# Kernel optimization log

Measured on AMD Instinct MI355X. Metric: run time of the kernel, lower is better.

The kernel has to match this reference:

```python
import jax, jax.numpy as jnp
import numpy as np

L, D, DB, P, B = 33, 2048, 1024, 24, 2048
EPS = 1e-5

def _ln(x, g, b):
    # LayerNorm over last axis, eps matches torch default 1e-5
    mu = jnp.mean(x, axis=-1, keepdims=True)
    var = jnp.mean(jnp.square(x - mu), axis=-1, keepdims=True)
    return (x - mu) * jax.lax.rsqrt(var + EPS) * g + b

def setup_inputs() -> dict:
    key = jax.random.key(0)
    ks = jax.random.split(key, 8)
    s1 = 1.0 / np.sqrt(D)   # fan-in style scaling to keep activations sane
    s2 = 1.0 / np.sqrt(DB)
    sp = 1.0 / np.sqrt(P)
    return {
        "x":      jax.random.normal(ks[0], (B, L, D), jnp.float32),
        "pos_emb": jax.random.uniform(ks[1], (L, P), jnp.float32),
        "Wk":     jax.random.normal(ks[2], (P, D), jnp.float32) * sp,
        "W1":     jax.random.normal(ks[3], (L, D, DB), jnp.float32) * s1,
        "b1":     jnp.zeros((L, DB), jnp.float32),
        "ln1_g":  jnp.ones((L, DB), jnp.float32),
        "ln1_b":  jnp.zeros((L, DB), jnp.float32),
        "W2":     jax.random.normal(ks[4], (L, DB, D), jnp.float32) * s2,
        "b2":     jnp.zeros((L, D), jnp.float32),
        "ln2_g":  jnp.ones((L, D), jnp.float32),
        "ln2_b":  jnp.zeros((L, D), jnp.float32),
        "Wq1":    jax.random.normal(ks[5], (D, DB), jnp.float32) * s1,
        "bq1":    jnp.zeros((DB,), jnp.float32),
        "lnq_g":  jnp.ones((DB,), jnp.float32),
        "lnq_b":  jnp.zeros((DB,), jnp.float32),
        "Wq2":    jax.random.normal(ks[6], (DB, D), jnp.float32) * s2,
        "bq2":    jnp.zeros((D,), jnp.float32),
    }

def reference(x, pos_emb, Wk, W1, b1, ln1_g, ln1_b, W2, b2, ln2_g, ln2_b,
              Wq1, bq1, lnq_g, lnq_b, Wq2, bq2):
    # x: [B, L, D]
    z_L = x[:, -1, :]                                   # [B, D]
    keys = pos_emb @ Wk                                 # Eq.10: [L, D]
    # Eq.11 + Eq.4: per-layer value MLPs, grouped as batched GEMMs
    h = jax.nn.gelu(jnp.einsum('bld,ldk->blk', x, W1) + b1, approximate=False)
    h = _ln(h, ln1_g, ln1_b)                            # [B, L, DB]
    v = jnp.einsum('blk,lkd->bld', h, W2) + b2          # [B, L, D]
    values = _ln(v, ln2_g, ln2_b)                       # [B, L, D]
    # Eq.5: query from last layer
    hq = jax.nn.gelu(z_L @ Wq1 + bq1, approximate=False)
    hq = _ln(hq, lnq_g, lnq_b)
    q_tr = hq @ Wq2 + bq2                               # [B, D]
    query = 1.0 + jax.nn.elu(z_L + q_tr)                # [B, D]
    # Eq.7-9: single-query attention over depth + residual
    attn = jax.nn.softmax(query @ keys.T, axis=-1)      # [B, L]
    attended = jnp.einsum('bl,bld->bd', attn, values)   # [B, D]
    return z_L + attended
```

## Files before the change

kernel.cpp:

```cpp
#include <hip/hip_runtime.h>
#include <cstddef>
#include <cstdint>

#define Lc 33
#define Dc 2048
#define DBc 1024
#define Pc 24
#define Bc 2048

typedef __attribute__((ext_vector_type(4))) float f32x4;
typedef __attribute__((ext_vector_type(8))) short s16x8;
typedef __attribute__((ext_vector_type(4))) short s16x4;

__device__ __forceinline__ short bf16r(float f) {
  unsigned u = __float_as_uint(f);
  u = (u + 0x7fffu + ((u >> 16) & 1u)) >> 16;
  return (short)u;
}
__device__ __forceinline__ float bf2f(short s) {
  return __uint_as_float(((unsigned)(unsigned short)s) << 16);
}
__device__ __forceinline__ s16x8 pack8(const float* f) {
  s16x8 r;
#pragma unroll
  for (int i = 0; i < 8; ++i) r[i] = bf16r(f[i]);
  return r;
}
__device__ __forceinline__ void split8(const float* f, s16x8& hi, s16x8& lo) {
#pragma unroll
  for (int i = 0; i < 8; ++i) {
    short h = bf16r(f[i]);
    hi[i] = h;
    lo[i] = bf16r(f[i] - bf2f(h));
  }
}
__device__ __forceinline__ void gl_lds16(const void* g, void* l) {
  __builtin_amdgcn_global_load_lds(
      (const __attribute__((address_space(1))) unsigned int*)g,
      (__attribute__((address_space(3))) unsigned int*)l, 16, 0, 0);
}

#define BARw() __builtin_amdgcn_s_barrier()
#define VM4() asm volatile("s_waitcnt vmcnt(4)" ::: "memory")

__global__ __launch_bounds__(256)
void cvt_bf16_kernel(const float* __restrict__ in,
                     unsigned short* __restrict__ outp) {
  const size_t i = ((size_t)blockIdx.x * 256 + threadIdx.x) * 8;
  f32x4 a = *(const f32x4*)(in + i);
  f32x4 b = *(const f32x4*)(in + i + 4);
  float f[8] = {a[0], a[1], a[2], a[3], b[0], b[1], b[2], b[3]};
  *(s16x8*)(outp + i) = pack8(f);
}

__global__ __launch_bounds__(256)
void keys_kernel(const float* __restrict__ pe, const float* __restrict__ Wk,
                 float* __restrict__ keys) {
  const int l = blockIdx.x;
  const int d = blockIdx.y * 256 + threadIdx.x;
  float s = 0.f;
#pragma unroll
  for (int p = 0; p < Pc; ++p) s += pe[l * Pc + p] * Wk[(size_t)p * Dc + d];
  keys[(size_t)l * Dc + d] = s;
}

template <int K, int N>
__global__ __launch_bounds__(256)
void transpose_w(const float* __restrict__ W, unsigned short* __restrict__ Wt) {
  const int z = blockIdx.z;
  const int k0 = blockIdx.x * 64, n0 = blockIdx.y * 64;
  __shared__ unsigned short tile[64][66];
  const int t = threadIdx.x;
  {
    const int r = t >> 2, cq = (t & 3) * 16;
    const float* src = W + (size_t)z * K * N + (size_t)(k0 + r) * N + n0 + cq;
#pragma unroll
    for (int i = 0; i < 16; i += 4) {
      f32x4 v = *(const f32x4*)(src + i);
#pragma unroll
      for (int j = 0; j < 4; ++j)
        tile[r][cq + i + j] = (unsigned short)bf16r(v[j]);
    }
  }
  __syncthreads();
  {
    const int n = t >> 2, kc = (t & 3) * 16;
    s16x8 o0, o1;
#pragma unroll
    for (int i = 0; i < 8; ++i) {
      o0[i] = tile[kc + i][n];
      o1[i] = tile[kc + 8 + i][n];
    }
    unsigned short* dst =
        Wt + (size_t)z * N * K + (size_t)(n0 + n) * K + k0 + kc;
    *(s16x8*)dst = o0;
    *(s16x8*)(dst + 8) = o1;
  }
}

template <int K, int N, int NBN, int GELU, int STATS>
__global__ __launch_bounds__(512, 2)
void gemm8ph(const unsigned short* __restrict__ A,
             const unsigned short* __restrict__ Wt,
             const float* __restrict__ bias,
             unsigned short* __restrict__ outbuf, float* __restrict__ stats) {
  constexpr int NT = K / 64;
  constexpr int NIT = NT / 2;
  constexpr int NBM = 8;
  extern __shared__ __align__(16) char smem[];

  constexpr int nwg = 33 * NBM * NBN;
  constexpr int q = nwg >> 3, r = nwg & 7;
  const int orig = blockIdx.x;
  const int xcd = orig & 7;
  const int wgid =
      ((xcd < r) ? xcd * (q + 1) : r * (q + 1) + (xcd - r) * q) + (orig >> 3);
  const int z = wgid / (NBM * NBN);
  const int rem = wgid - z * (NBM * NBN);
  const int bm = rem / NBN, bn = rem - bm * NBN;

  const int tid = threadIdx.x, lane = tid & 63, wv = tid >> 6;
  const int wm = wv >> 2, wn = wv & 3;
  const int wr = wm * 128, wc = wn * 64;
  const int l15 = lane & 15, l4 = lane >> 4;

  f32x4 acc[8][4];
#pragma unroll
  for (int m = 0; m < 8; ++m)
#pragma unroll
    for (int n = 0; n < 4; ++n) {
      acc[m][n][0] = 0.f; acc[m][n][1] = 0.f;
      acc[m][n][2] = 0.f; acc[m][n][3] = 0.f;
    }

  const unsigned short* aRow[2];
  const unsigned short* bRow[2];
  {
    const unsigned short* Bbase = Wt + (size_t)z * N * K;
#pragma unroll
    for (int c = 0; c < 2; ++c) {
      const int rprime = wv * 16 + c * 8 + (lane >> 3);
      const int row = 2 * rprime + ((lane >> 2) & 1);
      const int chunk = (lane & 3) ^ (rprime & 3);
      aRow[c] = A + (size_t)(bm * 256 + row) * ((size_t)Lc * K) +
                (size_t)z * K + chunk * 8;
      bRow[c] = Bbase + (size_t)(bn * 256 + row) * K + chunk * 8;
    }
  }

  auto STAGE_A = [&](int t, int kh) {
    char* dst = smem + (t & 1) * 65536 + kh * 16384 + wv * 2048;
    const int ko = t * 64 + kh * 32;
#pragma unroll
    for (int c = 0; c < 2; ++c) gl_lds16(aRow[c] + ko, dst + c * 1024);
  };
  auto STAGE_B = [&](int t, int kh) {
    char* dst = smem + (t & 1) * 65536 + 32768 + kh * 16384 + wv * 2048;
    const int ko = t * 64 + kh * 32;
#pragma unroll
    for (int c = 0; c < 2; ++c) gl_lds16(bRow[c] + ko, dst + c * 1024);
  };
  s16x8 afr[4], bfr[4];
  auto LDA = [&](int d, int kh, int mh) {
#pragma unroll
    for (int m = 0; m < 4; ++m) {
      const int row = wr + (mh * 4 + m) * 16 + l15;
      const int rp = row >> 1;
      afr[m] = *(const s16x8*)(smem + d * 65536 + kh * 16384 + rp * 128 +
                               (row & 1) * 64 + ((l4 ^ (rp & 3)) << 4));
    }
  };
  auto LDB = [&](int d, int kh) {
#pragma unroll
    for (int n = 0; n < 4; ++n) {
      const int row = wc + n * 16 + l15;
      const int rp = row >> 1;
      bfr[n] = *(const s16x8*)(smem + d * 65536 + 32768 + kh * 16384 +
                               rp * 128 + (row & 1) * 64 +
                               ((l4 ^ (rp & 3)) << 4));
    }
  };

#define MFMA16(MH)                                                          \
  {                                                                         \
    __builtin_amdgcn_s_setprio(1);                                          \
    _Pragma("unroll") for (int m_ = 0; m_ < 4; ++m_) {                      \
      _Pragma("unroll") for (int n_ = 0; n_ < 4; ++n_) {                    \
        acc[(MH) * 4 + m_][n_] = __builtin_amdgcn_mfma_f32_16x16x32_bf16(   \
            afr[m_], bfr[n_], acc[(MH) * 4 + m_][n_], 0, 0, 0);             \
      }                                                                     \
    }                                                                       \
    __builtin_amdgcn_s_setprio(0);                                          \
  }

  STAGE_A(0, 0); STAGE_B(0, 0); STAGE_A(0, 1); STAGE_B(0, 1);
  STAGE_A(1, 0); STAGE_B(1, 0);
  VM4();
  BARw();

  for (int i = 0; i < NIT; ++i) {
    const int t0 = 2 * i, t1 = 2 * i + 1;
    LDA(0, 0, 0); LDB(0, 0);
    STAGE_A(t1, 1);
    BARw(); MFMA16(0); BARw();
    LDA(0, 0, 1);
    STAGE_B(t1, 1);
    BARw(); MFMA16(1); BARw();
    LDA(0, 1, 0); LDB(0, 1);
    if (t0 + 2 < NT) STAGE_A(t0 + 2, 0);
    BARw(); MFMA16(0); BARw();
    LDA(0, 1, 1);
    if (t0 + 2 < NT) STAGE_B(t0 + 2, 0);
    BARw(); MFMA16(1);
    VM4();
    BARw();
    LDA(1, 0, 0); LDB(1, 0);
    if (t0 + 2 < NT) STAGE_A(t0 + 2, 1);
    BARw(); MFMA16(0); BARw();
    LDA(1, 0, 1);
    if (t0 + 2 < NT) STAGE_B(t0 + 2, 1);
    BARw(); MFMA16(1); BARw();
    LDA(1, 1, 0); LDB(1, 1);
    if (t0 + 3 < NT) STAGE_A(t0 + 3, 0);
    BARw(); MFMA16(0); BARw();
    LDA(1, 1, 1);
    if (t0 + 3 < NT) STAGE_B(t0 + 3, 0);
    BARw(); MFMA16(1);
    VM4();
    BARw();
  }
#undef MFMA16

  const float* biasP = bias + (size_t)z * N;
  float bsv[4];
#pragma unroll
  for (int n = 0; n < 4; ++n) bsv[n] = biasP[bn * 256 + wc + n * 16 + l15];

#pragma unroll
  for (int m = 0; m < 8; ++m) {
#pragma unroll
    for (int j = 0; j < 4; ++j) {
      const int grow = bm * 256 + wr + m * 16 + l4 * 4 + j;
      float s1 = 0.f, s2 = 0.f;
#pragma unroll
      for (int n = 0; n < 4; ++n) {
        const int col = bn * 256 + wc + n * 16 + l15;
        float v = acc[m][n][j] + bsv[n];
        if constexpr (GELU) v = 0.5f * v * (1.0f + erff(v * 0.70710678118f));
        outbuf[((size_t)grow * Lc + z) * N + col] = (unsigned short)bf16r(v);
        if constexpr (STATS) {
          s1 += v;
          s2 += v * v;
        }
      }
      if constexpr (STATS) {
#pragma unroll
        for (int o = 1; o < 16; o <<= 1) {
          s1 += __shfl_xor(s1, o);
          s2 += __shfl_xor(s2, o);
        }
        if (l15 == 0) {
          atomicAdd(&stats[((size_t)grow * Lc + z) * 2 + 0], s1);
          atomicAdd(&stats[((size_t)grow * Lc + z) * 2 + 1], s2);
        }
      }
    }
  }
}

template <int K, int N, int GELU>
__global__ __launch_bounds__(256, 2)
void gemm2ph(const unsigned short* __restrict__ A,
             const unsigned short* __restrict__ Wt,
             const float* __restrict__ bias,
             unsigned short* __restrict__ outbuf) {
  constexpr int NT = K / 64;
  const int z = blockIdx.z, bm = blockIdx.x, bn = blockIdx.y;
  const int tid = threadIdx.x, lane = tid & 63, w = tid >> 6;
  const int wr = (w >> 1) * 64, wc = (w & 1) * 64;
  const int l15 = lane & 15, kb = lane >> 4;

  __shared__ __align__(16) unsigned short Als[2][128 * 64];
  __shared__ __align__(16) unsigned short Bls[2][128 * 64];

  f32x4 acc[4][4];
#pragma unroll
  for (int m = 0; m < 4; ++m)
#pragma unroll
    for (int n = 0; n < 4; ++n) {
      acc[m][n][0] = 0.f; acc[m][n][1] = 0.f;
      acc[m][n][2] = 0.f; acc[m][n][3] = 0.f;
    }

  const int rl8 = lane >> 3, sl = lane & 7;
  const int swzE = ((sl ^ rl8) << 3);
  const unsigned short* Bbase = Wt + (size_t)z * N * K;

  auto stage = [&](int buf, int kt) {
#pragma unroll
    for (int j = 0; j < 4; ++j) {
      const int rloc = w * 32 + j * 8 + rl8;
      gl_lds16(A + ((size_t)(bm * 128 + rloc) * Lc + z) * K + kt * 64 + swzE,
               (char*)&Als[buf][0] + w * 4096 + j * 1024);
      gl_lds16(Bbase + (size_t)(bn * 128 + rloc) * K + kt * 64 + swzE,
               (char*)&Bls[buf][0] + w * 4096 + j * 1024);
    }
  };

  stage(0, 0);
  asm volatile("s_waitcnt vmcnt(0)" ::: "memory");
  __builtin_amdgcn_s_barrier();

  for (int kt = 0; kt < NT; ++kt) {
    const int cur = kt & 1;
    if (kt + 1 < NT) stage(cur ^ 1, kt + 1);
#pragma unroll
    for (int kk = 0; kk < 2; ++kk) {
      s16x8 af[4], bfv[4];
#pragma unroll
      for (int m = 0; m < 4; ++m) {
        const int row = wr + m * 16 + l15;
        const int slot = kk * 4 + kb;
        af[m] = *(const s16x8*)((const char*)&Als[cur][0] + row * 128 +
                                ((slot ^ (row & 7)) << 4));
      }
#pragma unroll
      for (int n = 0; n < 4; ++n) {
        const int row = wc + n * 16 + l15;
        const int slot = kk * 4 + kb;
        bfv[n] = *(const s16x8*)((const char*)&Bls[cur][0] + row * 128 +
                                 ((slot ^ (row & 7)) << 4));
      }
#pragma unroll
      for (int m = 0; m < 4; ++m)
#pragma unroll
        for (int n = 0; n < 4; ++n)
          acc[m][n] = __builtin_amdgcn_mfma_f32_16x16x32_bf16(
              af[m], bfv[n], acc[m][n], 0, 0, 0);
    }
    asm volatile("s_waitcnt vmcnt(0)" ::: "memory");
    __builtin_amdgcn_s_barrier();
  }

  const float* biasP = bias + (size_t)z * N;
#pragma unroll
  for (int m = 0; m < 4; ++m) {
    const int r0 = bm * 128 + wr + m * 16 + kb * 4;
#pragma unroll
    for (int n = 0; n < 4; ++n) {
      const int col = bn * 128 + wc + n * 16 + l15;
      const float bs = biasP[col];
#pragma unroll
      for (int j = 0; j < 4; ++j) {
        const int r = r0 + j;
        float v = acc[m][n][j] + bs;
        if constexpr (GELU) v = 0.5f * v * (1.0f + erff(v * 0.70710678118f));
        outbuf[((size_t)r * Lc + z) * N + col] = (unsigned short)bf16r(v);
      }
    }
  }
}

template <int MODE, int SPLITQ>
__global__ __launch_bounds__(256, 2)
void gemm_fused(const float* __restrict__ x,
                const unsigned short* __restrict__ hbuf,
                const float* __restrict__ hqF,
                const float* __restrict__ Wmain, const float* __restrict__ Wq,
                const float* __restrict__ bmain, const float* __restrict__ bq,
                unsigned short* __restrict__ outH, float* __restrict__ outHq,
                unsigned short* __restrict__ outV, float* __restrict__ outQ) {
  constexpr int K = (MODE == 1) ? 2048 : 1024;
  constexpr int N = (MODE == 1) ? 1024 : 2048;
  constexpr int BK = 32;
  constexpr int NT = K / BK;

  const int z = blockIdx.z;
  const int bm = blockIdx.x;
  const int bn = blockIdx.y;
  const int tid = threadIdx.x;
  const int lane = tid & 63;
  const int wid = tid >> 6;
  const int wr = (wid >> 1) * 64;
  const int wc = (wid & 1) * 64;
  const int l15 = lane & 15;
  const int kb = lane >> 4;

  const float* Bp = SPLITQ ? Wq : (Wmain + (size_t)z * K * N);

  __shared__ short Als[1 + SPLITQ][128][32];
  __shared__ short Bls[1 + SPLITQ][128][32];

  const f32x4 vzero = {0.f, 0.f, 0.f, 0.f};
  f32x4 acc[4][4];
#pragma unroll
  for (int m = 0; m < 4; ++m)
#pragma unroll
    for (int n = 0; n < 4; ++n) acc[m][n] = vzero;

  const int ar = tid >> 1;
  const int ak = (tid & 1) * 16;
  const int grow = bm * 128 + ar;

  const float* ApF = nullptr;
  const unsigned short* ApH = nullptr;
  if constexpr (MODE == 1) {
    const int lsel = SPLITQ ? (Lc - 1) : z;
    ApF = x + (size_t)grow * (Lc * Dc) + (size_t)lsel * Dc + ak;
  } else if constexpr (SPLITQ == 1) {
    ApF = hqF + (size_t)grow * DBc + ak;
  } else {
    ApH = hbuf + ((size_t)grow * 33 + z) * DBc + ak;
  }

  const int bnL = tid & 127;
  const int bj = tid >> 7;
  const int c0 = ((bnL >> 1) & 3) ^ bj;
  const int kc0 = c0 * 8;
  const int kc1 = (c0 ^ 2) * 8;
  const float* Bcol = Bp + (size_t)bn * 128 + bnL;

  float aF[16];
  s16x8 aH0, aH1;
  float bF[16];

  auto loadA = [&](int kt) {
    if constexpr (MODE == 2 && SPLITQ == 0) {
      const unsigned short* p = ApH + kt * BK;
      aH0 = *(const s16x8*)p;
      aH1 = *(const s16x8*)(p + 8);
    } else {
      const float* p = ApF + kt * BK;
#pragma unroll
      for (int i = 0; i < 4; ++i) {
        f32x4 t = *(const f32x4*)(p + i * 4);
#pragma unroll
        for (int j = 0; j < 4; ++j) aF[i * 4 + j] = t[j];
      }
    }
  };
  auto loadB = [&](int kt) {
    const float* p0 = Bcol + (size_t)(kt * BK + kc0) * N;
    const float* p1 = Bcol + (size_t)(kt * BK + kc1) * N;
#pragma unroll
    for (int i = 0; i < 8; ++i) bF[i] = p0[(size_t)i * N];
#pragma unroll
    for (int i = 0; i < 8; ++i) bF[8 + i] = p1[(size_t)i * N];
  };
  auto writeLDS = [&]() {
    if constexpr (MODE == 2 && SPLITQ == 0) {
      *(s16x8*)&Als[0][ar][ak] = aH0;
      *(s16x8*)&Als[0][ar][ak + 8] = aH1;
    } else if constexpr (SPLITQ == 0) {
      *(s16x8*)&Als[0][ar][ak] = pack8(aF);
      *(s16x8*)&Als[0][ar][ak + 8] = pack8(aF + 8);
    } else {
      s16x8 h0, l0, h1, l1;
      split8(aF, h0, l0);
      split8(aF + 8, h1, l1);
      *(s16x8*)&Als[0][ar][ak] = h0;
      *(s16x8*)&Als[1][ar][ak] = l0;
      *(s16x8*)&Als[0][ar][ak + 8] = h1;
      *(s16x8*)&Als[1][ar][ak + 8] = l1;
    }
    if constexpr (SPLITQ == 0) {
      *(s16x8*)&Bls[0][bnL][kc0] = pack8(bF);
      *(s16x8*)&Bls[0][bnL][kc1] = pack8(bF + 8);
    } else {
      s16x8 h0, l0, h1, l1;
      split8(bF, h0, l0);
      split8(bF + 8, h1, l1);
      *(s16x8*)&Bls[0][bnL][kc0] = h0;
      *(s16x8*)&Bls[1][bnL][kc0] = l0;
      *(s16x8*)&Bls[0][bnL][kc1] = h1;
      *(s16x8*)&Bls[1][bnL][kc1] = l1;
    }
  };

  loadA(0);
  loadB(0);
  for (int kt = 0; kt < NT; ++kt) {
    __syncthreads();
    writeLDS();
    if (kt + 1 < NT) {
      loadA(kt + 1);
      loadB(kt + 1);
    }
    __syncthreads();
    s16x8 af[4], bfv[4];
#pragma unroll
    for (int m = 0; m < 4; ++m)
      af[m] = *(const s16x8*)&Als[0][wr + m * 16 + l15][kb * 8];
#pragma unroll
    for (int n = 0; n < 4; ++n)
      bfv[n] = *(const s16x8*)&Bls[0][wc + n * 16 + l15][kb * 8];
    if constexpr (SPLITQ == 1) {
      s16x8 afl[4], bfl[4];
#pragma unroll
      for (int m = 0; m < 4; ++m)
        afl[m] = *(const s16x8*)&Als[1][wr + m * 16 + l15][kb * 8];
#pragma unroll
      for (int n = 0; n < 4; ++n)
        bfl[n] = *(const s16x8*)&Bls[1][wc + n * 16 + l15][kb * 8];
#pragma unroll
      for (int m = 0; m < 4; ++m)
#pragma unroll
        for (int n = 0; n < 4; ++n) {
          acc[m][n] = __builtin_amdgcn_mfma_f32_16x16x32_bf16(
              af[m], bfv[n], acc[m][n], 0, 0, 0);
          acc[m][n] = __builtin_amdgcn_mfma_f32_16x16x32_bf16(
              af[m], bfl[n], acc[m][n], 0, 0, 0);
          acc[m][n] = __builtin_amdgcn_mfma_f32_16x16x32_bf16(
              afl[m], bfv[n], acc[m][n], 0, 0, 0);
        }
    } else {
#pragma unroll
      for (int m = 0; m < 4; ++m)
#pragma unroll
        for (int n = 0; n < 4; ++n)
          acc[m][n] = __builtin_amdgcn_mfma_f32_16x16x32_bf16(
              af[m], bfv[n], acc[m][n], 0, 0, 0);
    }
  }

  const float* biasP = SPLITQ ? bq : (bmain + (size_t)z * N);
#pragma unroll
  for (int m = 0; m < 4; ++m) {
    const int r0 = bm * 128 + wr + m * 16 + kb * 4;
#pragma unroll
    for (int n = 0; n < 4; ++n) {
      const int col = bn * 128 + wc + n * 16 + l15;
      const float bs = biasP[col];
#pragma unroll
      for (int j = 0; j < 4; ++j) {
        const int r = r0 + j;
        const float v = acc[m][n][j] + bs;
        if constexpr (MODE == 1 && SPLITQ == 0) {
          const float g = 0.5f * v * (1.0f + erff(v * 0.70710678118f));
          outH[((size_t)r * 33 + z) * DBc + col] = (unsigned short)bf16r(g);
        } else if constexpr (MODE == 1 && SPLITQ == 1) {
          const float g = 0.5f * v * (1.0f + erff(v * 0.70710678118f));
          outHq[(size_t)r * DBc + col] = g;
        } else if constexpr (MODE == 2 && SPLITQ == 0) {
          outV[((size_t)r * 33 + z) * Dc + col] = (unsigned short)bf16r(v);
        } else {
          const float zl =
              x[(size_t)r * (Lc * Dc) + (size_t)(Lc - 1) * Dc + col];
          const float t = zl + v;
          outQ[(size_t)r * Dc + col] = (t > 0.f) ? (1.f + t) : __expf(t);
        }
      }
    }
  }
}

template <int W>
__global__ __launch_bounds__(256)
void ln_kernel(unsigned short* __restrict__ buf, const float* __restrict__ gmain,
               const float* __restrict__ bmain) {
  constexpr int E = W / 256;
  const int z = blockIdx.x;
  const int b = blockIdx.y;
  const int tid = threadIdx.x;
  unsigned short* row = buf + ((size_t)b * 33 + z) * W;
  float v[E];
  if constexpr (E == 4) {
    s16x4 t = *(const s16x4*)(row + tid * 4);
#pragma unroll
    for (int i = 0; i < 4; ++i) v[i] = bf2f(t[i]);
  } else {
    s16x8 t = *(const s16x8*)(row + tid * 8);
#pragma unroll
    for (int i = 0; i < 8; ++i) v[i] = bf2f(t[i]);
  }
  float s = 0.f, s2 = 0.f;
#pragma unroll
  for (int i = 0; i < E; ++i) {
    s += v[i];
    s2 += v[i] * v[i];
  }
#pragma unroll
  for (int o = 32; o > 0; o >>= 1) {
    s += __shfl_xor(s, o);
    s2 += __shfl_xor(s2, o);
  }
  __shared__ float red[2][4];
  const int w = tid >> 6;
  if ((tid & 63) == 0) {
    red[0][w] = s;
    red[1][w] = s2;
  }
  __syncthreads();
  s = red[0][0] + red[0][1] + red[0][2] + red[0][3];
  s2 = red[1][0] + red[1][1] + red[1][2] + red[1][3];
  const float mu = s * (1.0f / W);
  const float var = s2 * (1.0f / W) - mu * mu;
  const float rstd = rsqrtf(var + 1e-5f);
  const float* G = gmain + (size_t)z * W;
  const float* Bt = bmain + (size_t)z * W;
  if constexpr (E == 4) {
    f32x4 gv = *(const f32x4*)(G + tid * 4);
    f32x4 bv = *(const f32x4*)(Bt + tid * 4);
    s16x4 o;
#pragma unroll
    for (int i = 0; i < 4; ++i)
      o[i] = bf16r((v[i] - mu) * rstd * gv[i] + bv[i]);
    *(s16x4*)(row + tid * 4) = o;
  } else {
    f32x4 g0 = *(const f32x4*)(G + tid * 8);
    f32x4 g1 = *(const f32x4*)(G + tid * 8 + 4);
    f32x4 b0 = *(const f32x4*)(Bt + tid * 8);
    f32x4 b1 = *(const f32x4*)(Bt + tid * 8 + 4);
    s16x8 o;
#pragma unroll
    for (int i = 0; i < 4; ++i) {
      o[i] = bf16r((v[i] - mu) * rstd * g0[i] + b0[i]);
      o[i + 4] = bf16r((v[i + 4] - mu) * rstd * g1[i] + b1[i]);
    }
    *(s16x8*)(row + tid * 8) = o;
  }
}

__global__ __launch_bounds__(256)
void stats_kernel(const unsigned short* __restrict__ vals,
                  float* __restrict__ stats) {
  const int z = blockIdx.x;
  const int b = blockIdx.y;
  const int tid = threadIdx.x;
  const unsigned short* row = vals + ((size_t)b * 33 + z) * Dc;
  s16x8 t = *(const s16x8*)(row + tid * 8);
  float s = 0.f, s2 = 0.f;
#pragma unroll
  for (int i = 0; i < 8; ++i) {
    float v = bf2f(t[i]);
    s += v;
    s2 += v * v;
  }
#pragma unroll
  for (int o = 32; o > 0; o >>= 1) {
    s += __shfl_xor(s, o);
    s2 += __shfl_xor(s2, o);
  }
  __shared__ float red[2][4];
  const int w = tid >> 6;
  if ((tid & 63) == 0) {
    red[0][w] = s;
    red[1][w] = s2;
  }
  __syncthreads();
  if (tid == 0) {
    stats[((size_t)b * 33 + z) * 2 + 0] =
        red[0][0] + red[0][1] + red[0][2] + red[0][3];
    stats[((size_t)b * 33 + z) * 2 + 1] =
        red[1][0] + red[1][1] + red[1][2] + red[1][3];
  }
}

__global__ __launch_bounds__(256)
void ln_f32_kernel(float* __restrict__ buf, const float* __restrict__ g,
                   const float* __restrict__ bb) {
  const int r = blockIdx.x;
  const int tid = threadIdx.x;
  float* row = buf + (size_t)r * DBc;
  f32x4 v = *(const f32x4*)(row + tid * 4);
  float s = 0.f, s2 = 0.f;
#pragma unroll
  for (int i = 0; i < 4; ++i) {
    s += v[i];
    s2 += v[i] * v[i];
  }
#pragma unroll
  for (int o = 32; o > 0; o >>= 1) {
    s += __shfl_xor(s, o);
    s2 += __shfl_xor(s2, o);
  }
  __shared__ float red[2][4];
  const int w = tid >> 6;
  if ((tid & 63) == 0) {
    red[0][w] = s;
    red[1][w] = s2;
  }
  __syncthreads();
  s = red[0][0] + red[0][1] + red[0][2] + red[0][3];
  s2 = red[1][0] + red[1][1] + red[1][2] + red[1][3];
  const float mu = s * (1.0f / DBc);
  const float var = s2 * (1.0f / DBc) - mu * mu;
  const float rstd = rsqrtf(var + 1e-5f);
  f32x4 gv = *(const f32x4*)(g + tid * 4);
  f32x4 bv = *(const f32x4*)(bb + tid * 4);
  f32x4 o;
#pragma unroll
  for (int i = 0; i < 4; ++i) o[i] = (v[i] - mu) * rstd * gv[i] + bv[i];
  *(f32x4*)(row + tid * 4) = o;
}

__global__ __launch_bounds__(256)
void attn_kernel(const float* __restrict__ x, const float* __restrict__ query,
                 const float* __restrict__ keys,
                 const unsigned short* __restrict__ vals,
                 const float* __restrict__ stats, const float* __restrict__ g2,
                 const float* __restrict__ b2ln, float* __restrict__ out) {
  const int b = blockIdx.x;
  const int tid = threadIdx.x;
  const int d0 = tid * 8;

  float qv[8];
  {
    f32x4 t0 = *(const f32x4*)(query + (size_t)b * Dc + d0);
    f32x4 t1 = *(const f32x4*)(query + (size_t)b * Dc + d0 + 4);
#pragma unroll
    for (int i = 0; i < 4; ++i) {
      qv[i] = t0[i];
      qv[i + 4] = t1[i];
    }
  }
  float s[33];
#pragma unroll
  for (int l = 0; l < 33; ++l) {
    const float* kp = keys + (size_t)l * Dc + d0;
    f32x4 k0 = *(const f32x4*)kp;
    f32x4 k1 = *(const f32x4*)(kp + 4);
    float t = 0.f;
#pragma unroll
    for (int i = 0; i < 4; ++i) t += qv[i] * k0[i] + qv[i + 4] * k1[i];
    s[l] = t;
  }
#pragma unroll
  for (int l = 0; l < 33; ++l) {
    float v = s[l];
#pragma unroll
    for (int o = 32; o > 0; o >>= 1) v += __shfl_xor(v, o);
    s[l] = v;
  }
  __shared__ float sred[4][33];
  __shared__ float sl[33];
  const int w = tid >> 6;
  if ((tid & 63) == 0) {
#pragma unroll
    for (int l = 0; l < 33; ++l) sred[w][l] = s[l];
  }
  __syncthreads();
  if (tid < 33)
    sl[tid] = sred[0][tid] + sred[1][tid] + sred[2][tid] + sred[3][tid];
  __syncthreads();

  float m = -1e30f;
#pragma unroll
  for (int l = 0; l < 33; ++l) m = fmaxf(m, sl[l]);
  float p[33];
  float sum = 0.f;
#pragma unroll
  for (int l = 0; l < 33; ++l) {
    p[l] = __expf(sl[l] - m);
    sum += p[l];
  }
  const float inv = 1.0f / sum;

  float acc8[8];
  {
    const float* zl = x + (size_t)b * (Lc * Dc) + (size_t)(Lc - 1) * Dc + d0;
    f32x4 z0 = *(const f32x4*)zl;
    f32x4 z1 = *(const f32x4*)(zl + 4);
#pragma unroll
    for (int i = 0; i < 4; ++i) {
      acc8[i] = z0[i];
      acc8[i + 4] = z1[i];
    }
  }
  const unsigned short* vb = vals + (size_t)b * 33 * Dc + d0;
#pragma unroll
  for (int l = 0; l < 33; ++l) {
    const float st0 = stats[((size_t)b * 33 + l) * 2 + 0];
    const float st1 = stats[((size_t)b * 33 + l) * 2 + 1];
    const float mu = st0 * (1.0f / Dc);
    const float var = st1 * (1.0f / Dc) - mu * mu;
    const float rstd = rsqrtf(var + 1e-5f);
    const float a = p[l] * inv;
    s16x8 vv = *(const s16x8*)(vb + (size_t)l * Dc);
    const float* gp = g2 + (size_t)l * Dc + d0;
    const float* bp = b2ln + (size_t)l * Dc + d0;
    f32x4 g0 = *(const f32x4*)gp, g1 = *(const f32x4*)(gp + 4);
    f32x4 b0 = *(const f32x4*)bp, b1 = *(const f32x4*)(bp + 4);
#pragma unroll
    for (int i = 0; i < 4; ++i) {
      acc8[i] += a * ((bf2f(vv[i]) - mu) * rstd * g0[i] + b0[i]);
      acc8[i + 4] += a * ((bf2f(vv[i + 4]) - mu) * rstd * g1[i] + b1[i]);
    }
  }
  f32x4 o0, o1;
#pragma unroll
  for (int i = 0; i < 4; ++i) {
    o0[i] = acc8[i];
    o1[i] = acc8[i + 4];
  }
  *(f32x4*)(out + (size_t)b * Dc + d0) = o0;
  *(f32x4*)(out + (size_t)b * Dc + d0 + 4) = o1;
}

extern "C" void kernel_launch(void* const* d_in, const int* in_sizes, int n_in,
                              void* d_out, int out_size, void* d_ws,
                              size_t ws_size, hipStream_t stream) {
  const float* x = (const float*)d_in[0];
  const float* pe = (const float*)d_in[1];
  const float* Wk = (const float*)d_in[2];
  const float* W1 = (const float*)d_in[3];
  const float* b1 = (const float*)d_in[4];
  const float* ln1g = (const float*)d_in[5];
  const float* ln1b = (const float*)d_in[6];
  const float* W2 = (const float*)d_in[7];
  const float* b2 = (const float*)d_in[8];
  const float* ln2g = (const float*)d_in[9];
  const float* ln2b = (const float*)d_in[10];
  const float* Wq1 = (const float*)d_in[11];
  const float* bq1 = (const float*)d_in[12];
  const float* lnqg = (const float*)d_in[13];
  const float* lnqb = (const float*)d_in[14];
  const float* Wq2 = (const float*)d_in[15];
  const float* bq2 = (const float*)d_in[16];
  float* out = (float*)d_out;
  char* ws = (char*)d_ws;

  float* keysP = (float*)(ws);
  float* queryP = (float*)(ws + 270336);
  float* hqP = (float*)(ws + 17047552);
  float* statsP = (float*)(ws + 25436160);
  unsigned short* hP = (unsigned short*)(ws + 25976832);
  unsigned short* xbfP = (unsigned short*)(ws + 164388864);
  unsigned short* valsP = (unsigned short*)(ws + 164388864);
  unsigned short* W1tP = (unsigned short*)(ws + 441212928);
  unsigned short* W2tP = (unsigned short*)(ws + 441212928);

  const bool fast = (ws_size >= 579624960ull);
  bool use8 = fast;
  if (fast) {
    if (hipFuncSetAttribute(
            reinterpret_cast<const void*>(&gemm8ph<2048, 1024, 4, 1, 0>),
            hipFuncAttributeMaxDynamicSharedMemorySize, 131072) != hipSuccess)
      use8 = false;
    if (hipFuncSetAttribute(
            reinterpret_cast<const void*>(&gemm8ph<1024, 2048, 8, 0, 1>),
            hipFuncAttributeMaxDynamicSharedMemorySize, 131072) != hipSuccess)
      use8 = false;
  }

  keys_kernel<<<dim3(33, 8), 256, 0, stream>>>(pe, Wk, keysP);

  gemm_fused<1, 1><<<dim3(16, 8, 1), 256, 0, stream>>>(
      x, nullptr, nullptr, nullptr, Wq1, nullptr, bq1, nullptr, hqP, nullptr,
      nullptr);

  if (fast) {
    cvt_bf16_kernel<<<dim3(67584), 256, 0, stream>>>(x, xbfP);
    transpose_w<2048, 1024><<<dim3(32, 16, 33), 256, 0, stream>>>(W1, W1tP);
    if (use8) {
      gemm8ph<2048, 1024, 4, 1, 0><<<dim3(33 * 8 * 4), 512, 131072, stream>>>(
          xbfP, W1tP, b1, hP, nullptr);
    } else {
      gemm2ph<2048, 1024, 1><<<dim3(16, 8, 33), 256, 0, stream>>>(xbfP, W1tP,
                                                                  b1, hP);
    }
  } else {
    gemm_fused<1, 0><<<dim3(16, 8, 33), 256, 0, stream>>>(
        x, nullptr, nullptr, W1, nullptr, b1, nullptr, hP, nullptr, nullptr,
        nullptr);
  }

  ln_kernel<1024><<<dim3(33, 2048), 256, 0, stream>>>(hP, ln1g, ln1b);

  ln_f32_kernel<<<dim3(2048), 256, 0, stream>>>(hqP, lnqg, lnqb);

  hipMemsetAsync(statsP, 0, 2048 * 33 * 2 * sizeof(float), stream);

  if (fast) {
    transpose_w<1024, 2048><<<dim3(16, 32, 33), 256, 0, stream>>>(W2, W2tP);
    if (use8) {
      gemm8ph<1024, 2048, 8, 0, 1><<<dim3(33 * 8 * 8), 512, 131072, stream>>>(
          hP, W2tP, b2, valsP, statsP);
    } else {
      gemm2ph<1024, 2048, 0><<<dim3(16, 16, 33), 256, 0, stream>>>(hP, W2tP,
                                                                   b2, valsP);
      stats_kernel<<<dim3(33, 2048), 256, 0, stream>>>(valsP, statsP);
    }
  } else {
    gemm_fused<2, 0><<<dim3(16, 16, 33), 256, 0, stream>>>(
        x, hP, nullptr, W2, nullptr, b2, nullptr, nullptr, nullptr, valsP,
        nullptr);
    stats_kernel<<<dim3(33, 2048), 256, 0, stream>>>(valsP, statsP);
  }

  gemm_fused<2, 1><<<dim3(16, 16, 1), 256, 0, stream>>>(
      x, nullptr, hqP, nullptr, Wq2, nullptr, bq2, nullptr, nullptr, nullptr,
      queryP);

  attn_kernel<<<dim3(2048), 256, 0, stream>>>(x, queryP, keysP, valsP, statsP,
                                              ln2g, ln2b, out);
}
```

Baseline: 1.603 ms.

## Fold LN1 into W2 GEMM epilogue and use layer-major activation layout

Instead of normalizing h in place with a separate LayerNorm pass, row statistics of h are computed by a light reduction kernel. The LN gain is folded into a pre-transposed W2, with column sums and bias terms precomputed so the second GEMM epilogue applies mean/rstd analytically. Activations switch to a layer-major [L,B,*] layout so GEMM A-tiles are contiguous, and the atomics-based stats epilogue is replaced by a separate stats pass with no memset. This removes a read-modify-write pass over h, at the cost of precision drift from variance-by-moments and bf16 scaling of g*W.

```diff
diff --git a/kernel.cpp b/kernel.cpp
--- a/kernel.cpp
+++ b/kernel.cpp
@@ -44,13 +44,15 @@
 #define VM4() asm volatile("s_waitcnt vmcnt(4)" ::: "memory")
 
 __global__ __launch_bounds__(256)
-void cvt_bf16_kernel(const float* __restrict__ in,
+void cvt_perm_kernel(const float* __restrict__ in,
                      unsigned short* __restrict__ outp) {
-  const size_t i = ((size_t)blockIdx.x * 256 + threadIdx.x) * 8;
-  f32x4 a = *(const f32x4*)(in + i);
-  f32x4 b = *(const f32x4*)(in + i + 4);
+  const int row = blockIdx.x, z = blockIdx.y;
+  const int k0 = threadIdx.x * 8;
+  const float* src = in + ((size_t)row * Lc + z) * Dc + k0;
+  f32x4 a = *(const f32x4*)(src);
+  f32x4 b = *(const f32x4*)(src + 4);
   float f[8] = {a[0], a[1], a[2], a[3], b[0], b[1], b[2], b[3]};
-  *(s16x8*)(outp + i) = pack8(f);
+  *(s16x8*)(outp + ((size_t)z * Bc + row) * Dc + k0) = pack8(f);
 }
 
 __global__ __launch_bounds__(256)
@@ -98,12 +100,121 @@
   }
 }
 
-template <int K, int N, int NBN, int GELU, int STATS>
+__global__ __launch_bounds__(256)
+void transpose_w2g(const float* __restrict__ W, const float* __restrict__ g,
+                   const float* __restrict__ bvec, const float* __restrict__ b2,
+                   unsigned short* __restrict__ Wt, float* __restrict__ gw,
+                   float* __restrict__ bw) {
+  constexpr int K = 1024, N = 2048;
+  const int z = blockIdx.y;
+  const int n0 = blockIdx.x * 64;
+  __shared__ unsigned short tileG[64][66];
+  __shared__ unsigned short tileW[64][66];
+  const int t = threadIdx.x;
+  const int rL = t >> 2, cq = (t & 3) * 16;
+  const int nS = t >> 2, kc = (t & 3) * 16;
+  float gwp = 0.f, bwp = 0.f;
+
+  for (int kt = 0; kt < 16; ++kt) {
+    {
+      const float gs = g[(size_t)z * K + kt * 64 + rL];
+      const float* src =
+          W + (size_t)z * K * N + (size_t)(kt * 64 + rL) * N + n0 + cq;
+#pragma unroll
+      for (int i = 0; i < 16; i += 4) {
+        f32x4 v = *(const f32x4*)(src + i);
+#pragma unroll
+        for (int j = 0; j < 4; ++j) {
+          tileW[rL][cq + i + j] = (unsigned short)bf16r(v[j]);
+          tileG[rL][cq + i + j] = (unsigned short)bf16r(gs * v[j]);
+        }
+      }
+    }
+    __syncthreads();
+    {
+      s16x8 o0, o1;
+#pragma unroll
+      for (int i = 0; i < 8; ++i) {
+        o0[i] = tileG[kc + i][nS];
+        o1[i] = tileG[kc + 8 + i][nS];
+      }
+#pragma unroll
+      for (int i = 0; i < 16; ++i) {
+        gwp += bf2f(tileG[kc + i][nS]);
+        bwp += bvec[(size_t)z * K + kt * 64 + kc + i] * bf2f(tileW[kc + i][nS]);
+      }
+      unsigned short* dst =
+          Wt + (size_t)z * N * K + (size_t)(n0 + nS) * K + kt * 64 + kc;
+      *(s16x8*)dst = o0;
+      *(s16x8*)(dst + 8) = o1;
+    }
+    __syncthreads();
+  }
+  gwp += __shfl_xor(gwp, 1);
+  gwp += __shfl_xor(gwp, 2);
+  bwp += __shfl_xor(bwp, 1);
+  bwp += __shfl_xor(bwp, 2);
+  if ((t & 3) == 0) {
+    gw[(size_t)z * N + n0 + nS] = gwp;
+    bw[(size_t)z * N + n0 + nS] = bwp + b2[(size_t)z * N + n0 + nS];
+  }
+}
+
+template <int W>
+__global__ __launch_bounds__(256)
+void stats_w_kernel(const unsigned short* __restrict__ buf,
+                    float* __restrict__ stats) {
+  constexpr int E = W / 256;
+  const int z = blockIdx.x;
+  const int b = blockIdx.y;
+  const int tid = threadIdx.x;
+  const unsigned short* row = buf + ((size_t)z * Bc + b) * W;
+  float s = 0.f, s2 = 0.f;
+  if constexpr (E == 4) {
+    s16x4 t = *(const s16x4*)(row + tid * 4);
+#pragma unroll
+    for (int i = 0; i < 4; ++i) {
+      float v = bf2f(t[i]);
+      s += v;
+      s2 += v * v;
+    }
+  } else {
+    s16x8 t = *(const s16x8*)(row + tid * 8);
+#pragma unroll
+    for (int i = 0; i < 8; ++i) {
+      float v = bf2f(t[i]);
+      s += v;
+      s2 += v * v;
+    }
+  }
+#pragma unroll
+  for (int o = 32; o > 0; o >>= 1) {
+    s += __shfl_xor(s, o);
+    s2 += __shfl_xor(s2, o);
+  }
+  __shared__ float red[2][4];
+  const int w = tid >> 6;
+  if ((tid & 63) == 0) {
+    red[0][w] = s;
+    red[1][w] = s2;
+  }
+  __syncthreads();
+  if (tid == 0) {
+    stats[((size_t)z * Bc + b) * 2 + 0] =
+        red[0][0] + red[0][1] + red[0][2] + red[0][3];
+    stats[((size_t)z * Bc + b) * 2 + 1] =
+        red[1][0] + red[1][1] + red[1][2] + red[1][3];
+  }
+}
+
+template <int K, int N, int NBN, int GELU, int FUSE>
 __global__ __launch_bounds__(512, 2)
 void gemm8ph(const unsigned short* __restrict__ A,
              const unsigned short* __restrict__ Wt,
              const float* __restrict__ bias,
-             unsigned short* __restrict__ outbuf, float* __restrict__ stats) {
+             unsigned short* __restrict__ outbuf,
+             const float* __restrict__ gw, const float* __restrict__ bw,
+             const float* __restrict__ stats1) {
   constexpr int NT = K / 64;
   constexpr int NIT = NT / 2;
   constexpr int NBM = 8;
@@ -142,8 +253,7 @@
       const int rprime = wv * 16 + c * 8 + (lane >> 3);
       const int row = 2 * rprime + ((lane >> 2) & 1);
       const int chunk = (lane & 3) ^ (rprime & 3);
-      aRow[c] = A + (size_t)(bm * 256 + row) * ((size_t)Lc * K) +
-                (size_t)z * K + chunk * 8;
+      aRow[c] = A + ((size_t)z * Bc + bm * 256 + row) * K + chunk * 8;
       bRow[c] = Bbase + (size_t)(bn * 256 + row) * K + chunk * 8;
     }
   }
@@ -231,131 +341,42 @@
   }
 #undef MFMA16
 
-  const float* biasP = bias + (size_t)z * N;
-  float bsv[4];
-#pragma unroll
-  for (int n = 0; n < 4; ++n) bsv[n] = biasP[bn * 256 + wc + n * 16 + l15];
+  float bsv[4], gwv[4], bwv[4];
+#pragma unroll
+  for (int n = 0; n < 4; ++n) {
+    const int col = bn * 256 + wc + n * 16 + l15;
+    if constexpr (FUSE) {
+      gwv[n] = gw[(size_t)z * N + col];
+      bwv[n] = bw[(size_t)z * N + col];
+    } else {
+      bsv[n] = bias[(size_t)z * N + col];
+    }
+  }
 
 #pragma unroll
   for (int m = 0; m < 8; ++m) {
 #pragma unroll
     for (int j = 0; j < 4; ++j) {
       const int grow = bm * 256 + wr + m * 16 + l4 * 4 + j;
-      float s1 = 0.f, s2 = 0.f;
+      float mu = 0.f, rstd = 0.f;
+      if constexpr (FUSE) {
+        const float st0 = stats1[((size_t)z * Bc + grow) * 2 + 0];
+        const float st1 = stats1[((size_t)z * Bc + grow) * 2 + 1];
+        mu = st0 * (1.0f / K);
+        const float var = st1 * (1.0f / K) - mu * mu;
+        rstd = rsqrtf(var + 1e-5f);
+      }
 #pragma unroll
       for (int n = 0; n < 4; ++n) {
         const int col = bn * 256 + wc + n * 16 + l15;
-        float v = acc[m][n][j] + bsv[n];
+        float v;
+        if constexpr (FUSE) {
+          v = rstd * acc[m][n][j] - (rstd * mu) * gwv[n] + bwv[n];
+        } else {
+          v = acc[m][n][j] + bsv[n];
+        }
         if constexpr (GELU) v = 0.5f * v * (1.0f + erff(v * 0.70710678118f));
-        outbuf[((size_t)grow * Lc + z) * N + col] = (unsigned short)bf16r(v);
-        if constexpr (STATS) {
-          s1 += v;
-          s2 += v * v;
-        }
-      }
-      if constexpr (STATS) {
-#pragma unroll
-        for (int o = 1; o < 16; o <<= 1) {
-          s1 += __shfl_xor(s1, o);
-          s2 += __shfl_xor(s2, o);
-        }
-        if (l15 == 0) {
-          atomicAdd(&stats[((size_t)grow * Lc + z) * 2 + 0], s1);
-          atomicAdd(&stats[((size_t)grow * Lc + z) * 2 + 1], s2);
-        }
-      }
-    }
-  }
-}
-
-template <int K, int N, int GELU>
-__global__ __launch_bounds__(256, 2)
-void gemm2ph(const unsigned short* __restrict__ A,
-             const unsigned short* __restrict__ Wt,
-             const float* __restrict__ bias,
-             unsigned short* __restrict__ outbuf) {
-  constexpr int NT = K / 64;
-  const int z = blockIdx.z, bm = blockIdx.x, bn = blockIdx.y;
-  const int tid = threadIdx.x, lane = tid & 63, w = tid >> 6;
-  const int wr = (w >> 1) * 64, wc = (w & 1) * 64;
-  const int l15 = lane & 15, kb = lane >> 4;
-
-  __shared__ __align__(16) unsigned short Als[2][128 * 64];
-  __shared__ __align__(16) unsigned short Bls[2][128 * 64];
-
-  f32x4 acc[4][4];
-#pragma unroll
-  for (int m = 0; m < 4; ++m)
-#pragma unroll
-    for (int n = 0; n < 4; ++n) {
-      acc[m][n][0] = 0.f; acc[m][n][1] = 0.f;
-      acc[m][n][2] = 0.f; acc[m][n][3] = 0.f;
-    }
-
-  const int rl8 = lane >> 3, sl = lane & 7;
-  const int swzE = ((sl ^ rl8) << 3);
-  const unsigned short* Bbase = Wt + (size_t)z * N * K;
-
-  auto stage = [&](int buf, int kt) {
-#pragma unroll
-    for (int j = 0; j < 4; ++j) {
-      const int rloc = w * 32 + j * 8 + rl8;
-      gl_lds16(A + ((size_t)(bm * 128 + rloc) * Lc + z) * K + kt * 64 + swzE,
-               (char*)&Als[buf][0] + w * 4096 + j * 1024);
-      gl_lds16(Bbase + (size_t)(bn * 128 + rloc) * K + kt * 64 + swzE,
-               (char*)&Bls[buf][0] + w * 4096 + j * 1024);
-    }
-  };
-
-  stage(0, 0);
-  asm volatile("s_waitcnt vmcnt(0)" ::: "memory");
-  __builtin_amdgcn_s_barrier();
-
-  for (int kt = 0; kt < NT; ++kt) {
-    const int cur = kt & 1;
-    if (kt + 1 < NT) stage(cur ^ 1, kt + 1);
-#pragma unroll
-    for (int kk = 0; kk < 2; ++kk) {
-      s16x8 af[4], bfv[4];
-#pragma unroll
-      for (int m = 0; m < 4; ++m) {
-        const int row = wr + m * 16 + l15;
-        const int slot = kk * 4 + kb;
-        af[m] = *(const s16x8*)((const char*)&Als[cur][0] + row * 128 +
-                                ((slot ^ (row & 7)) << 4));
-      }
-#pragma unroll
-      for (int n = 0; n < 4; ++n) {
-        const int row = wc + n * 16 + l15;
-        const int slot = kk * 4 + kb;
-        bfv[n] = *(const s16x8*)((const char*)&Bls[cur][0] + row * 128 +
-                                 ((slot ^ (row & 7)) << 4));
-      }
-#pragma unroll
-      for (int m = 0; m < 4; ++m)
-#pragma unroll
-        for (int n = 0; n < 4; ++n)
-          acc[m][n] = __builtin_amdgcn_mfma_f32_16x16x32_bf16(
-              af[m], bfv[n], acc[m][n], 0, 0, 0);
-    }
-    asm volatile("s_waitcnt vmcnt(0)" ::: "memory");
-    __builtin_amdgcn_s_barrier();
-  }
-
-  const float* biasP = bias + (size_t)z * N;
-#pragma unroll
-  for (int m = 0; m < 4; ++m) {
-    const int r0 = bm * 128 + wr + m * 16 + kb * 4;
-#pragma unroll
-    for (int n = 0; n < 4; ++n) {
-      const int col = bn * 128 + wc + n * 16 + l15;
-      const float bs = biasP[col];
-#pragma unroll
-      for (int j = 0; j < 4; ++j) {
-        const int r = r0 + j;
-        float v = acc[m][n][j] + bs;
-        if constexpr (GELU) v = 0.5f * v * (1.0f + erff(v * 0.70710678118f));
-        outbuf[((size_t)r * Lc + z) * N + col] = (unsigned short)bf16r(v);
+        outbuf[((size_t)z * Bc + grow) * N + col] = (unsigned short)bf16r(v);
       }
     }
   }
@@ -410,7 +431,7 @@
   } else if constexpr (SPLITQ == 1) {
     ApF = hqF + (size_t)grow * DBc + ak;
   } else {
-    ApH = hbuf + ((size_t)grow * 33 + z) * DBc + ak;
+    ApH = hbuf + ((size_t)z * Bc + grow) * DBc + ak;
   }
 
   const int bnL = tid & 127;
@@ -537,12 +558,12 @@
         const float v = acc[m][n][j] + bs;
         if constexpr (MODE == 1 && SPLITQ == 0) {
           const float g = 0.5f * v * (1.0f + erff(v * 0.70710678118f));
-          outH[((size_t)r * 33 + z) * DBc + col] = (unsigned short)bf16r(g);
+          outH[((size_t)z * Bc + r) * DBc + col] = (unsigned short)bf16r(g);
         } else if constexpr (MODE == 1 && SPLITQ == 1) {
           const float g = 0.5f * v * (1.0f + erff(v * 0.70710678118f));
           outHq[(size_t)r * DBc + col] = g;
         } else if constexpr (MODE == 2 && SPLITQ == 0) {
-          outV[((size_t)r * 33 + z) * Dc + col] = (unsigned short)bf16r(v);
+          outV[((size_t)z * Bc + r) * Dc + col] = (unsigned short)bf16r(v);
         } else {
           const float zl =
               x[(size_t)r * (Lc * Dc) + (size_t)(Lc - 1) * Dc + col];
@@ -562,7 +583,7 @@
   const int z = blockIdx.x;
   const int b = blockIdx.y;
   const int tid = threadIdx.x;
-  unsigned short* row = buf + ((size_t)b * 33 + z) * W;
+  unsigned short* row = buf + ((size_t)z * Bc + b) * W;
   float v[E];
   if constexpr (E == 4) {
     s16x4 t = *(const s16x4*)(row + tid * 4);
@@ -622,41 +643,6 @@
 }
 
 __global__ __launch_bounds__(256)
-void stats_kernel(const unsigned short* __restrict__ vals,
-                  float* __restrict__ stats) {
-  const int z = blockIdx.x;
-  const int b = blockIdx.y;
-  const int tid = threadIdx.x;
-  const unsigned short* row = vals + ((size_t)b * 33 + z) * Dc;
-  s16x8 t = *(const s16x8*)(row + tid * 8);
-  float s = 0.f, s2 = 0.f;
-#pragma unroll
-  for (int i = 0; i < 8; ++i) {
-    float v = bf2f(t[i]);
-    s += v;
-    s2 += v * v;
-  }
-#pragma unroll
-  for (int o = 32; o > 0; o >>= 1) {
-    s += __shfl_xor(s, o);
-    s2 += __shfl_xor(s2, o);
-  }
-  __shared__ float red[2][4];
-  const int w = tid >> 6;
-  if ((tid & 63) == 0) {
-    red[0][w] = s;
-    red[1][w] = s2;
-  }
-  __syncthreads();
-  if (tid == 0) {
-    stats[((size_t)b * 33 + z) * 2 + 0] =
-        red[0][0] + red[0][1] + red[0][2] + red[0][3];
-    stats[((size_t)b * 33 + z) * 2 + 1] =
-        red[1][0] + red[1][1] + red[1][2] + red[1][3];
-  }
-}
-
-__global__ __launch_bounds__(256)
 void ln_f32_kernel(float* __restrict__ buf, const float* __restrict__ g,
                    const float* __restrict__ bb) {
   const int r = blockIdx.x;
@@ -767,16 +753,15 @@
       acc8[i + 4] = z1[i];
     }
   }
-  const unsigned short* vb = vals + (size_t)b * 33 * Dc + d0;
 #pragma unroll
   for (int l = 0; l < 33; ++l) {
-    const float st0 = stats[((size_t)b * 33 + l) * 2 + 0];
-    const float st1 = stats[((size_t)b * 33 + l) * 2 + 1];
+    const float st0 = stats[((size_t)l * Bc + b) * 2 + 0];
+    const float st1 = stats[((size_t)l * Bc + b) * 2 + 1];
     const float mu = st0 * (1.0f / Dc);
     const float var = st1 * (1.0f / Dc) - mu * mu;
     const float rstd = rsqrtf(var + 1e-5f);
     const float a = p[l] * inv;
-    s16x8 vv = *(const s16x8*)(vb + (size_t)l * Dc);
+    s16x8 vv = *(const s16x8*)(vals + ((size_t)l * Bc + b) * Dc + d0);
     const float* gp = g2 + (size_t)l * Dc + d0;
     const float* bp = b2ln + (size_t)l * Dc + d0;
     f32x4 g0 = *(const f32x4*)gp, g1 = *(const f32x4*)(gp + 4);
@@ -823,14 +808,17 @@
   float* keysP = (float*)(ws);
   float* queryP = (float*)(ws + 270336);
   float* hqP = (float*)(ws + 17047552);
-  float* statsP = (float*)(ws + 25436160);
-  unsigned short* hP = (unsigned short*)(ws + 25976832);
-  unsigned short* xbfP = (unsigned short*)(ws + 164388864);
-  unsigned short* valsP = (unsigned short*)(ws + 164388864);
-  unsigned short* W1tP = (unsigned short*)(ws + 441212928);
-  unsigned short* W2tP = (unsigned short*)(ws + 441212928);
-
-  const bool fast = (ws_size >= 579624960ull);
+  float* stats1P = (float*)(ws + 25436160);
+  float* stats2P = (float*)(ws + 25976832);
+  float* gwP = (float*)(ws + 26517504);
+  float* bwP = (float*)(ws + 26787840);
+  unsigned short* hP = (unsigned short*)(ws + 27058176);
+  unsigned short* xbfP = (unsigned short*)(ws + 165470208);
+  unsigned short* valsP = (unsigned short*)(ws + 165470208);
+  unsigned short* W1tP = (unsigned short*)(ws + 442294272);
+  unsigned short* W2gtP = (unsigned short*)(ws + 442294272);
+
+  const bool fast = (ws_size >= 580706304ull);
   bool use8 = fast;
   if (fast) {
     if (hipFuncSetAttribute(
@@ -849,49 +837,36 @@
       x, nullptr, nullptr, nullptr, Wq1, nullptr, bq1, nullptr, hqP, nullptr,
       nullptr);
 
-  if (fast) {
-    cvt_bf16_kernel<<<dim3(67584), 256, 0, stream>>>(x, xbfP);
+  if (use8) {
+    cvt_perm_kernel<<<dim3(2048, 33), 256, 0, stream>>>(x, xbfP);
     transpose_w<2048, 1024><<<dim3(32, 16, 33), 256, 0, stream>>>(W1, W1tP);
-    if (use8) {
-      gemm8ph<2048, 1024, 4, 1, 0><<<dim3(33 * 8 * 4), 512, 131072, stream>>>(
-          xbfP, W1tP, b1, hP, nullptr);
-    } else {
-      gemm2ph<2048, 1024, 1><<<dim3(16, 8, 33), 256, 0, stream>>>(xbfP, W1tP,
-                                                                  b1, hP);
-    }
+    gemm8ph<2048, 1024, 4, 1, 0>
+        <<<dim3(33 * 8 * 4), 512, 131072, stream>>>(xbfP, W1tP, b1, hP,
+                                                    nullptr, nullptr, nullptr);
+    stats_w_kernel<1024><<<dim3(33, 2048), 256, 0, stream>>>(hP, stats1P);
+    ln_f32_kernel<<<dim3(2048), 256, 0, stream>>>(hqP, lnqg, lnqb);
+    transpose_w2g<<<dim3(32, 33), 256, 0, stream>>>(W2, ln1g, ln1b, b2, W2gtP,
+                                                    gwP, bwP);
+    gemm8ph<1024, 2048, 8, 0, 1>
+        <<<dim3(33 * 8 * 8), 512, 131072, stream>>>(hP, W2gtP, nullptr, valsP,
+                                                    gwP, bwP, stats1P);
+    stats_w_kernel<2048><<<dim3(33, 2048), 256, 0, stream>>>(valsP, stats2P);
   } else {
     gemm_fused<1, 0><<<dim3(16, 8, 33), 256, 0, stream>>>(
         x, nullptr, nullptr, W1, nullptr, b1, nullptr, hP, nullptr, nullptr,
         nullptr);
-  }
-
-  ln_kernel<1024><<<dim3(33, 2048), 256, 0, stream>>>(hP, ln1g, ln1b);
-
-  ln_f32_kernel<<<dim3(2048), 256, 0, stream>>>(hqP, lnqg, lnqb);
-
-  hipMemsetAsync(statsP, 0, 2048 * 33 * 2 * sizeof(float), stream);
-
-  if (fast) {
-    transpose_w<1024, 2048><<<dim3(16, 32, 33), 256, 0, stream>>>(W2, W2tP);
-    if (use8) {
-      gemm8ph<1024, 2048, 8, 0, 1><<<dim3(33 * 8 * 8), 512, 131072, stream>>>(
-          hP, W2tP, b2, valsP, statsP);
-    } else {
-      gemm2ph<1024, 2048, 0><<<dim3(16, 16, 33), 256, 0, stream>>>(hP, W2tP,
-                                                                   b2, valsP);
-      stats_kernel<<<dim3(33, 2048), 256, 0, stream>>>(valsP, statsP);
-    }
-  } else {
+    ln_kernel<1024><<<dim3(33, 2048), 256, 0, stream>>>(hP, ln1g, ln1b);
+    ln_f32_kernel<<<dim3(2048), 256, 0, stream>>>(hqP, lnqg, lnqb);
     gemm_fused<2, 0><<<dim3(16, 16, 33), 256, 0, stream>>>(
         x, hP, nullptr, W2, nullptr, b2, nullptr, nullptr, nullptr, valsP,
         nullptr);
-    stats_kernel<<<dim3(33, 2048), 256, 0, stream>>>(valsP, statsP);
+    stats_w_kernel<2048><<<dim3(33, 2048), 256, 0, stream>>>(valsP, stats2P);
   }
 
   gemm_fused<2, 1><<<dim3(16, 16, 1), 256, 0, stream>>>(
       x, nullptr, hqP, nullptr, Wq2, nullptr, bq2, nullptr, nullptr, nullptr,
       queryP);
 
-  attn_kernel<<<dim3(2048), 256, 0, stream>>>(x, queryP, keysP, valsP, statsP,
-                                              ln2g, ln2b, out);
-}
+  attn_kernel<<<dim3(2048), 256, 0, stream>>>(x, queryP, keysP, valsP,
+                                              stats2P, ln2g, ln2b, out);
+}
```

Result: faster. 1.529 ms, median of 2 (-4.6%).
